# Performance work log

Measured on AMD Instinct MI355X. Metric: run time of the kernel, lower is better.

Reference implementation:

```python
import jax, jax.numpy as jnp
import numpy as np

N_EMBD = 768
N_HEAD = 12


def setup_inputs() -> dict:
    key = jax.random.key(0)
    ks = jax.random.split(key, 5)
    B, T, C = 8, 1024, N_EMBD
    s_in = 1.0 / np.sqrt(C)
    x = jax.random.normal(ks[0], (B, T, C), dtype=jnp.float32)
    w_attn = jax.random.normal(ks[1], (C, 3 * C), dtype=jnp.float32) * s_in
    b_attn = jnp.zeros((3 * C,), dtype=jnp.float32)
    w_proj = jax.random.normal(ks[2], (C, C), dtype=jnp.float32) * s_in
    b_proj = jnp.zeros((C,), dtype=jnp.float32)
    return {"x": x, "w_attn": w_attn, "b_attn": b_attn,
            "w_proj": w_proj, "b_proj": b_proj}


def reference(x, w_attn, b_attn, w_proj, b_proj):
    B, T, C = x.shape
    H, hs = N_HEAD, C // N_HEAD
    qkv = x @ w_attn + b_attn                      # [B,T,3C]
    q, k, v = jnp.split(qkv, 3, axis=-1)
    # [B,H,T,hs]
    q = q.reshape(B, T, H, hs).transpose(0, 2, 1, 3)
    k = k.reshape(B, T, H, hs).transpose(0, 2, 1, 3)
    v = v.reshape(B, T, H, hs).transpose(0, 2, 1, 3)
    att = jnp.einsum('bhqd,bhkd->bhqk', q, k) * (1.0 / np.sqrt(hs))
    causal = jnp.tril(jnp.ones((T, T), dtype=bool))
    att = jnp.where(causal, att, -jnp.inf)
    att = jax.nn.softmax(att, axis=-1)
    y = jnp.einsum('bhqk,bhkd->bhqd', att, v)      # [B,H,T,hs]
    y = y.transpose(0, 2, 1, 3).reshape(B, T, C)
    return y @ w_proj + b_proj
```

## Files before the change

### kernel.cpp

```cpp
#include <hip/hip_runtime.h>
#include <hip/hip_bf16.h>
#include <stdint.h>

typedef unsigned short u16;
typedef short short8 __attribute__((ext_vector_type(8)));
typedef short short4v __attribute__((ext_vector_type(4)));
typedef float floatx4 __attribute__((ext_vector_type(4)));

__device__ __forceinline__ float b2f(u16 v) {
  union { unsigned int u; float f; } c; c.u = ((unsigned int)v) << 16; return c.f;
}
__device__ __forceinline__ u16 f2b(float f) {
  union { float f; unsigned int u; } c; c.f = f;
  unsigned int u = c.u;
  return (u16)((u + 0x7fffu + ((u >> 16) & 1u)) >> 16);
}

__device__ __forceinline__ void gld_lds16(const u16* g, u16* l) {
  __builtin_amdgcn_global_load_lds(
      (const __attribute__((address_space(1))) unsigned int*)g,
      (__attribute__((address_space(3))) unsigned int*)l,
      16, 0, 0);
}

__device__ __forceinline__ void tile_transpose_f2b(
    const float* __restrict__ in, u16* __restrict__ out,
    int inRS, int outRS, int rb, int cb, int tid)
{
  __shared__ __align__(16) u16 t[64][72];
  const int r = tid >> 2, sg = tid & 3;
  const float* ip = in + (long)(rb + r) * inRS + cb + sg * 16;
#pragma unroll
  for (int i = 0; i < 16; i += 4) {
    float4 f = *(const float4*)(ip + i);
    t[r][sg * 16 + i]     = f2b(f.x);
    t[r][sg * 16 + i + 1] = f2b(f.y);
    t[r][sg * 16 + i + 2] = f2b(f.z);
    t[r][sg * 16 + i + 3] = f2b(f.w);
  }
  __syncthreads();
  short8 v0, v1;
#pragma unroll
  for (int i = 0; i < 8; i++) v0[i] = (short)t[sg * 16 + i][r];
#pragma unroll
  for (int i = 0; i < 8; i++) v1[i] = (short)t[sg * 16 + 8 + i][r];
  *(short8*)(out + (long)(cb + r) * outRS + rb + sg * 16)     = v0;
  *(short8*)(out + (long)(cb + r) * outRS + rb + sg * 16 + 8) = v1;
}

__global__ __launch_bounds__(256) void prep(
    const float* __restrict__ x, u16* __restrict__ xb,
    const float* __restrict__ w_attn, u16* __restrict__ wTa,
    const float* __restrict__ w_proj, u16* __restrict__ wTp)
{
  const int bid = blockIdx.x, tid = threadIdx.x;
  if (bid < 6144) {
    int i = (bid * 256 + tid) * 4;
    float4 f = *(const float4*)(x + i);
    short4v v;
    v[0] = (short)f2b(f.x); v[1] = (short)f2b(f.y);
    v[2] = (short)f2b(f.z); v[3] = (short)f2b(f.w);
    *(short4v*)(xb + i) = v;
  } else if (bid < 6576) {
    int t = bid - 6144;
    tile_transpose_f2b(w_attn, wTa, 2304, 768, (t / 36) * 64, (t % 36) * 64, tid);
  } else {
    int t = bid - 6576;
    tile_transpose_f2b(w_proj, wTp, 768, 768, (t / 12) * 64, (t % 12) * 64, tid);
  }
}

__device__ __forceinline__ void store_out(u16* p, float v)  { *p = f2b(v); }
__device__ __forceinline__ void store_out(float* p, float v) { *p = v; }

template <int BM>
__device__ __forceinline__ void stage(
    const u16* __restrict__ A, const u16* __restrict__ Bt,
    long rowbase, long colbase, int K, int k0,
    u16* dA, u16* dB, int tid)
{
  const int c0 = tid, c1 = tid + 256;
  const int ar0 = c0 >> 2, ak0 = (c0 & 3) * 8;
  const int ar1 = c1 >> 2, ak1 = (c1 & 3) * 8;
  gld_lds16(A + (rowbase + ar0) * K + k0 + ak0, dA + c0 * 8);
  if (BM == 128)
    gld_lds16(A + (rowbase + ar1) * K + k0 + ak1, dA + c1 * 8);
  gld_lds16(Bt + (colbase + ar0) * K + k0 + ak0, dB + c0 * 8);
  gld_lds16(Bt + (colbase + ar1) * K + k0 + ak1, dB + c1 * 8);
}

template <typename OT, int BM>
__global__ __launch_bounds__(256) void gemm_bt_bias(
    const u16* __restrict__ A, const u16* __restrict__ Bt,
    const float* __restrict__ bias, OT* __restrict__ C,
    int M, int N, int K)
{
  constexpr int WNF = (BM == 128) ? 4 : 2;
  __shared__ __align__(16) u16 sA[2][BM * 32];
  __shared__ __align__(16) u16 sB[2][128 * 32];
  const int tid = threadIdx.x;
  const int lane = tid & 63;
  const int wave = tid >> 6;
  const int wm = (BM == 128) ? (wave >> 1) * 64 : 0;
  const int wn = (BM == 128) ? (wave & 1) * 64 : wave * 32;
  const int l15 = lane & 15;
  const int q = lane >> 4;
  const long rowbase = (long)blockIdx.y * BM;
  const long colbase = (long)blockIdx.x * 128;

  floatx4 acc[4][WNF];
#pragma unroll
  for (int i = 0; i < 4; i++)
#pragma unroll
    for (int j = 0; j < WNF; j++) acc[i][j] = (floatx4){0.f, 0.f, 0.f, 0.f};

  stage<BM>(A, Bt, rowbase, colbase, K, 0, sA[0], sB[0], tid);
  __syncthreads();

  const int NIT = K / 32;
  for (int it = 0; it < NIT; ++it) {
    const int cur = it & 1;
    if (it + 1 < NIT)
      stage<BM>(A, Bt, rowbase, colbase, K, (it + 1) * 32, sA[cur ^ 1], sB[cur ^ 1], tid);
    short8 af[4], bf[WNF];
#pragma unroll
    for (int mt = 0; mt < 4; mt++)
      af[mt] = *(const short8*)(sA[cur] + (wm + mt * 16 + l15) * 32 + q * 8);
#pragma unroll
    for (int nt = 0; nt < WNF; nt++)
      bf[nt] = *(const short8*)(sB[cur] + (wn + nt * 16 + l15) * 32 + q * 8);
#pragma unroll
    for (int mt = 0; mt < 4; mt++)
#pragma unroll
      for (int nt = 0; nt < WNF; nt++)
        acc[mt][nt] = __builtin_amdgcn_mfma_f32_16x16x32_bf16(af[mt], bf[nt], acc[mt][nt], 0, 0, 0);
    if (it + 1 < NIT) __syncthreads();
  }

#pragma unroll
  for (int nt = 0; nt < WNF; nt++) {
    const long col = colbase + wn + nt * 16 + l15;
    const float bv = bias[col];
#pragma unroll
    for (int mt = 0; mt < 4; mt++)
#pragma unroll
      for (int r = 0; r < 4; r++) {
        const long row = rowbase + wm + mt * 16 + q * 4 + r;
        store_out(C + row * N + col, acc[mt][nt][r] + bv);
      }
  }
}

__global__ __launch_bounds__(256) void attn_fwd(
    const u16* __restrict__ qkv, u16* __restrict__ y)
{
  const int bh = blockIdx.x;
  const int qt = 15 - blockIdx.y;
  const int b = bh / 12, h = bh % 12;
  const long rowOff = (long)b * 1024;
  const int qb = qt * 64;

  __shared__ __align__(16) u16 sK[64 * 72];
  __shared__ __align__(16) u16 sVs[64 * 72];
  __shared__ __align__(16) u16 sV[64 * 72];
  __shared__ __align__(16) u16 sP[64 * 72];

  const int tid = threadIdx.x;
  const int lane = tid & 63, wave = tid >> 6;
  const int l15 = lane & 15, q = lane >> 4;
  const int qrow_g = qb + wave * 16 + l15;

  short8 qf[2];
  {
    const u16* qp = qkv + (long)(rowOff + qrow_g) * 2304 + h * 64 + q * 8;
    short8 a0 = *(const short8*)(qp);
    short8 a1 = *(const short8*)(qp + 32);
#pragma unroll
    for (int i = 0; i < 8; i++) {
      a0[i] = (short)f2b(b2f((u16)a0[i]) * 0.125f);
      a1[i] = (short)f2b(b2f((u16)a1[i]) * 0.125f);
    }
    qf[0] = a0; qf[1] = a1;
  }

  float m_i = -1e30f, l_i = 0.f;
  floatx4 o[4];
#pragma unroll
  for (int nt = 0; nt < 4; nt++) o[nt] = (floatx4){0.f, 0.f, 0.f, 0.f};

  for (int j = 0; j <= qt; j++) {
    const int jb = j * 64;
#pragma unroll
    for (int rep = 0; rep < 2; rep++) {
      int idx = tid + rep * 256;
      int r = idx >> 3, ch = (idx & 7) * 8;
      const u16* src = qkv + (long)(rowOff + jb + r) * 2304 + 768 + h * 64 + ch;
      *(short8*)(sK + r * 72 + ch)  = *(const short8*)(src);
      *(short8*)(sVs + r * 72 + ch) = *(const short8*)(src + 768);
    }
    __syncthreads();

    {
      int d = tid >> 2, kg = (tid & 3) * 16;
      u16 tmp[16];
#pragma unroll
      for (int i = 0; i < 16; i++) tmp[i] = sVs[(kg + i) * 72 + d];
#pragma unroll
      for (int s = 0; s < 4; s++) {
        short4v vv;
        vv[0] = (short)tmp[s*4]; vv[1] = (short)tmp[s*4+1];
        vv[2] = (short)tmp[s*4+2]; vv[3] = (short)tmp[s*4+3];
        *(short4v*)(sV + d * 72 + kg + s * 4) = vv;
      }
    }

    floatx4 sf[4];
#pragma unroll
    for (int mt = 0; mt < 4; mt++) sf[mt] = (floatx4){0.f, 0.f, 0.f, 0.f};
#pragma unroll
    for (int kk = 0; kk < 2; kk++) {
#pragma unroll
      for (int mt = 0; mt < 4; mt++) {
        short8 kf = *(const short8*)(sK + (mt * 16 + l15) * 72 + kk * 32 + q * 8);
        sf[mt] = __builtin_amdgcn_mfma_f32_16x16x32_bf16(kf, qf[kk], sf[mt], 0, 0, 0);
      }
    }

    float mx = m_i;
#pragma unroll
    for (int mt = 0; mt < 4; mt++)
#pragma unroll
      for (int r = 0; r < 4; r++) {
        int key_g = jb + mt * 16 + q * 4 + r;
        float v = sf[mt][r];
        if (key_g > qrow_g) v = -1e30f;
        sf[mt][r] = v;
        mx = fmaxf(mx, v);
      }
    mx = fmaxf(mx, __shfl_xor(mx, 16));
    mx = fmaxf(mx, __shfl_xor(mx, 32));
    float al = __expf(m_i - mx);
    m_i = mx;
    float rsum = 0.f;
#pragma unroll
    for (int mt = 0; mt < 4; mt++) {
      short4v pv;
#pragma unroll
      for (int r = 0; r < 4; r++) {
        float p = __expf(sf[mt][r] - mx);
        rsum += p;
        pv[r] = (short)f2b(p);
      }
      *(short4v*)(sP + (wave * 16 + l15) * 72 + mt * 16 + q * 4) = pv;
    }
    rsum += __shfl_xor(rsum, 16);
    rsum += __shfl_xor(rsum, 32);
    l_i = l_i * al + rsum;
    __syncthreads();

    float al_r[4];
#pragma unroll
    for (int r = 0; r < 4; r++) al_r[r] = __shfl(al, q * 4 + r);
#pragma unroll
    for (int nt = 0; nt < 4; nt++)
#pragma unroll
      for (int r = 0; r < 4; r++) o[nt][r] *= al_r[r];
#pragma unroll
    for (int kk = 0; kk < 2; kk++) {
      short8 pf = *(const short8*)(sP + (wave * 16 + l15) * 72 + kk * 32 + q * 8);
#pragma unroll
      for (int nt = 0; nt < 4; nt++) {
        short8 vf = *(const short8*)(sV + (nt * 16 + l15) * 72 + kk * 32 + q * 8);
        o[nt] = __builtin_amdgcn_mfma_f32_16x16x32_bf16(pf, vf, o[nt], 0, 0, 0);
      }
    }
  }

  float linv = 1.f / l_i;
  float li_r[4];
#pragma unroll
  for (int r = 0; r < 4; r++) li_r[r] = __shfl(linv, q * 4 + r);
#pragma unroll
  for (int nt = 0; nt < 4; nt++)
#pragma unroll
    for (int r = 0; r < 4; r++) {
      int row = qb + wave * 16 + q * 4 + r;
      int col = h * 64 + nt * 16 + l15;
      y[(rowOff + row) * 768 + col] = f2b(o[nt][r] * li_r[r]);
    }
}

extern "C" void kernel_launch(void* const* d_in, const int* in_sizes, int n_in,
                              void* d_out, int out_size, void* d_ws, size_t ws_size,
                              hipStream_t stream) {
  const float* x      = (const float*)d_in[0];
  const float* w_attn = (const float*)d_in[1];
  const float* b_attn = (const float*)d_in[2];
  const float* w_proj = (const float*)d_in[3];
  const float* b_proj = (const float*)d_in[4];
  float* out = (float*)d_out;

  char* ws = (char*)d_ws;
  u16* xb   = (u16*)ws; ws += (size_t)8192 * 768 * 2;
  u16* wTa  = (u16*)ws; ws += (size_t)2304 * 768 * 2;
  u16* wTp  = (u16*)ws; ws += (size_t)768 * 768 * 2;
  u16* qkv  = (u16*)ws; ws += (size_t)8192 * 2304 * 2;
  u16* yatt = (u16*)ws; ws += (size_t)8192 * 768 * 2;

  prep<<<dim3(6720), 256, 0, stream>>>(x, xb, w_attn, wTa, w_proj, wTp);

  gemm_bt_bias<u16, 128><<<dim3(18, 64), 256, 0, stream>>>(xb, wTa, b_attn, qkv, 8192, 2304, 768);

  attn_fwd<<<dim3(96, 16), 256, 0, stream>>>(qkv, yatt);

  gemm_bt_bias<float, 64><<<dim3(6, 128), 256, 0, stream>>>(yatt, wTp, b_proj, out, 8192, 768, 768);
}
```

Before: 221.8 us.

## Write V transposed from QKV GEMM epilogue and drop in-attention LDS transpose

The QKV GEMM epilogue now writes the V third of its output directly in a per-head transposed [b,h,d,t] layout, while Q and K go to a narrower buffer. The attention kernel then loads V^T tiles straight into LDS, removing the per-tile LDS transpose pass, and double-buffers sV by iteration parity. The cost is strided 8-byte global stores in the GEMM epilogue for the V columns, and a second sV buffer in LDS.

```diff
diff --git a/kernel.cpp b/kernel.cpp
--- a/kernel.cpp
+++ b/kernel.cpp
@@ -89,11 +89,11 @@
   gld_lds16(Bt + (colbase + ar1) * K + k0 + ak1, dB + c1 * 8);
 }
 
-template <typename OT, int BM>
+template <typename OT, int BM, bool SPLIT>
 __global__ __launch_bounds__(256) void gemm_bt_bias(
     const u16* __restrict__ A, const u16* __restrict__ Bt,
-    const float* __restrict__ bias, OT* __restrict__ C,
-    int M, int N, int K)
+    const float* __restrict__ bias, OT* __restrict__ C, u16* __restrict__ vT,
+    int M, int N, int K, int strideC)
 {
   constexpr int WNF = (BM == 128) ? 4 : 2;
   __shared__ __align__(16) u16 sA[2][BM * 32];
@@ -137,22 +137,41 @@
     if (it + 1 < NIT) __syncthreads();
   }
 
-#pragma unroll
-  for (int nt = 0; nt < WNF; nt++) {
-    const long col = colbase + wn + nt * 16 + l15;
-    const float bv = bias[col];
-#pragma unroll
-    for (int mt = 0; mt < 4; mt++)
-#pragma unroll
-      for (int r = 0; r < 4; r++) {
-        const long row = rowbase + wm + mt * 16 + q * 4 + r;
-        store_out(C + row * N + col, acc[mt][nt][r] + bv);
-      }
+  if (SPLIT && colbase >= 1536) {
+    const long b = rowbase >> 10;
+    const int t0b = (int)(rowbase & 1023) + wm;
+#pragma unroll
+    for (int nt = 0; nt < WNF; nt++) {
+      const int col = (int)colbase + wn + nt * 16 + l15;
+      const float bv = bias[col];
+      const int dloc = col - 1536;
+      u16* bp = vT + (b * 12 + (dloc >> 6)) * 65536L + (long)(dloc & 63) * 1024;
+#pragma unroll
+      for (int mt = 0; mt < 4; mt++) {
+        short4v pv;
+#pragma unroll
+        for (int r = 0; r < 4; r++) pv[r] = (short)f2b(acc[mt][nt][r] + bv);
+        *(short4v*)(bp + t0b + mt * 16 + q * 4) = pv;
+      }
+    }
+  } else {
+#pragma unroll
+    for (int nt = 0; nt < WNF; nt++) {
+      const long col = colbase + wn + nt * 16 + l15;
+      const float bv = bias[col];
+#pragma unroll
+      for (int mt = 0; mt < 4; mt++)
+#pragma unroll
+        for (int r = 0; r < 4; r++) {
+          const long row = rowbase + wm + mt * 16 + q * 4 + r;
+          store_out(C + row * strideC + col, acc[mt][nt][r] + bv);
+        }
+    }
   }
 }
 
 __global__ __launch_bounds__(256) void attn_fwd(
-    const u16* __restrict__ qkv, u16* __restrict__ y)
+    const u16* __restrict__ qk, const u16* __restrict__ vT, u16* __restrict__ y)
 {
   const int bh = blockIdx.x;
   const int qt = 15 - blockIdx.y;
@@ -161,8 +180,7 @@
   const int qb = qt * 64;
 
   __shared__ __align__(16) u16 sK[64 * 72];
-  __shared__ __align__(16) u16 sVs[64 * 72];
-  __shared__ __align__(16) u16 sV[64 * 72];
+  __shared__ __align__(16) u16 sV[2][64 * 72];
   __shared__ __align__(16) u16 sP[64 * 72];
 
   const int tid = threadIdx.x;
@@ -172,7 +190,7 @@
 
   short8 qf[2];
   {
-    const u16* qp = qkv + (long)(rowOff + qrow_g) * 2304 + h * 64 + q * 8;
+    const u16* qp = qk + (long)(rowOff + qrow_g) * 1536 + h * 64 + q * 8;
     short8 a0 = *(const short8*)(qp);
     short8 a1 = *(const short8*)(qp + 32);
 #pragma unroll
@@ -190,29 +208,17 @@
 
   for (int j = 0; j <= qt; j++) {
     const int jb = j * 64;
+    u16* sVc = sV[j & 1];
 #pragma unroll
     for (int rep = 0; rep < 2; rep++) {
       int idx = tid + rep * 256;
       int r = idx >> 3, ch = (idx & 7) * 8;
-      const u16* src = qkv + (long)(rowOff + jb + r) * 2304 + 768 + h * 64 + ch;
-      *(short8*)(sK + r * 72 + ch)  = *(const short8*)(src);
-      *(short8*)(sVs + r * 72 + ch) = *(const short8*)(src + 768);
+      *(short8*)(sK + r * 72 + ch) =
+          *(const short8*)(qk + (long)(rowOff + jb + r) * 1536 + 768 + h * 64 + ch);
+      *(short8*)(sVc + r * 72 + ch) =
+          *(const short8*)(vT + (long)bh * 65536 + (long)r * 1024 + jb + ch);
     }
     __syncthreads();
-
-    {
-      int d = tid >> 2, kg = (tid & 3) * 16;
-      u16 tmp[16];
-#pragma unroll
-      for (int i = 0; i < 16; i++) tmp[i] = sVs[(kg + i) * 72 + d];
-#pragma unroll
-      for (int s = 0; s < 4; s++) {
-        short4v vv;
-        vv[0] = (short)tmp[s*4]; vv[1] = (short)tmp[s*4+1];
-        vv[2] = (short)tmp[s*4+2]; vv[3] = (short)tmp[s*4+3];
-        *(short4v*)(sV + d * 72 + kg + s * 4) = vv;
-      }
-    }
 
     floatx4 sf[4];
 #pragma unroll
@@ -270,7 +276,7 @@
       short8 pf = *(const short8*)(sP + (wave * 16 + l15) * 72 + kk * 32 + q * 8);
 #pragma unroll
       for (int nt = 0; nt < 4; nt++) {
-        short8 vf = *(const short8*)(sV + (nt * 16 + l15) * 72 + kk * 32 + q * 8);
+        short8 vf = *(const short8*)(sVc + (nt * 16 + l15) * 72 + kk * 32 + q * 8);
         o[nt] = __builtin_amdgcn_mfma_f32_16x16x32_bf16(pf, vf, o[nt], 0, 0, 0);
       }
     }
@@ -304,14 +310,17 @@
   u16* xb   = (u16*)ws; ws += (size_t)8192 * 768 * 2;
   u16* wTa  = (u16*)ws; ws += (size_t)2304 * 768 * 2;
   u16* wTp  = (u16*)ws; ws += (size_t)768 * 768 * 2;
-  u16* qkv  = (u16*)ws; ws += (size_t)8192 * 2304 * 2;
+  u16* qk   = (u16*)ws; ws += (size_t)8192 * 1536 * 2;
+  u16* vT   = (u16*)ws; ws += (size_t)96 * 64 * 1024 * 2;
   u16* yatt = (u16*)ws; ws += (size_t)8192 * 768 * 2;
 
   prep<<<dim3(6720), 256, 0, stream>>>(x, xb, w_attn, wTa, w_proj, wTp);
 
-  gemm_bt_bias<u16, 128><<<dim3(18, 64), 256, 0, stream>>>(xb, wTa, b_attn, qkv, 8192, 2304, 768);
-
-  attn_fwd<<<dim3(96, 16), 256, 0, stream>>>(qkv, yatt);
-
-  gemm_bt_bias<float, 64><<<dim3(6, 128), 256, 0, stream>>>(yatt, wTp, b_proj, out, 8192, 768, 768);
-}
+  gemm_bt_bias<u16, 128, true><<<dim3(18, 64), 256, 0, stream>>>(
+      xb, wTa, b_attn, qk, vT, 8192, 2304, 768, 1536);
+
+  attn_fwd<<<dim3(96, 16), 256, 0, stream>>>(qk, vT, yatt);
+
+  gemm_bt_bias<float, 64, false><<<dim3(6, 128), 256, 0, stream>>>(
+      yatt, wTp, b_proj, out, (u16*)nullptr, 8192, 768, 768, 768);
+}
```

Measured after the change: 211.6 us. 1.05x faster.
